# Optimization experiments

Hardware: AMD Instinct MI355X
Metric: run time of the kernel (lower is better)

Reference implementation:

```python
import jax, jax.numpy as jnp
import numpy as np

LEVELS = np.array([8, 5, 5, 5], dtype=np.int64)
BASIS = np.cumprod(np.concatenate([[1], LEVELS[:-1]])).astype(np.int64)  # [1,8,40,200]
N_E = int(np.prod(LEVELS))  # 1000
BN_EPS = 1e-5
BOUND_EPS = 1e-3


def setup_inputs() -> dict:
    key = jax.random.key(0)
    ks = jax.random.split(key, 3)
    B, C, T, E = 32, 512, 4096, 4
    return {
        "z": jax.random.normal(ks[0], (B, C, T), dtype=jnp.float32),
        "W_in": jax.random.normal(ks[1], (C, E), dtype=jnp.float32) * 0.05,
        "b_in": jnp.zeros((E,), dtype=jnp.float32),
        "gamma": jnp.ones((E,), dtype=jnp.float32),
        "beta": jnp.zeros((E,), dtype=jnp.float32),
        "W_out": jax.random.normal(ks[2], (E, C), dtype=jnp.float32) * 0.05,
        "b_out": jnp.zeros((C,), dtype=jnp.float32),
    }


def _round_ste(x):
    return x + jax.lax.stop_gradient(jnp.round(x) - x)


def reference(z, W_in, b_in, gamma, beta, W_out, b_out):
    levels = jnp.asarray(LEVELS, dtype=jnp.float32)      # [E]
    basis = jnp.asarray(BASIS, dtype=jnp.float32)        # [E]
    half_w = jnp.floor(levels / 2.0)                     # levels // 2
    B, C, T = z.shape
    N = B * T

    # preprocess: 'n c t -> (n t) c'
    x = jnp.transpose(z, (0, 2, 1)).reshape(N, C)        # [N, C]
    # project_in
    h = x @ W_in + b_in                                   # [N, E]
    # BatchNorm1d, training mode (biased batch stats)
    mu = jnp.mean(h, axis=0)
    var = jnp.var(h, axis=0)
    h = (h - mu) * jax.lax.rsqrt(var + BN_EPS) * gamma + beta

    # bound + round_ste quantize
    half_l = (levels - 1.0) * (1.0 - BOUND_EPS) / 2.0
    offset = jnp.where(jnp.mod(levels, 2.0) == 0.0, 0.5, 0.0)
    shift = jnp.tan(offset / half_l)
    bounded = jnp.tanh(h + shift) * half_l - offset
    zhat_n = _round_ste(bounded) / half_w                 # [N, E], normalized codes

    # codes -> indices
    idx = jnp.sum((zhat_n * half_w + half_w) * basis, axis=-1).astype(jnp.int32)  # [N]

    # project_out, '(b t) c -> b c t'
    out = zhat_n @ W_out + b_out                          # [N, C]
    zhat = jnp.transpose(out.reshape(B, T, C), (0, 2, 1))  # [B, C, T]

    commit_loss = jnp.mean((z - jax.lax.stop_gradient(zhat)) ** 2)

    # perplexity via counts (avoids [N, n_e] one-hot)
    counts = jnp.zeros((N_E,), dtype=jnp.float32).at[idx].add(1.0)
    e_mean = counts / N
    perplexity = jnp.exp(-jnp.sum(e_mean * jnp.log(e_mean + 1e-10)))

    return zhat, commit_loss, perplexity
```

## Files before the change

kernel.cpp:

```cpp
#include <hip/hip_runtime.h>
#include <math.h>


namespace {
constexpr int Cv = 512, Tv = 4096, Bv = 32;
constexpr int Nv = Bv * Tv;
constexpr long long TOTv = (long long)Nv * Cv;
constexpr int NBA = 512;
constexpr int NBC = 512;
constexpr int NCP = 128;

constexpr size_t OFF_H  = 0;
constexpr size_t OFF_G  = OFF_H  + (size_t)Nv * 16;
constexpr size_t OFF_BS = OFF_G  + (size_t)Nv * 16;
constexpr size_t OFF_CN = OFF_BS + (size_t)NBA * 10 * 8;
constexpr size_t OFF_CP = OFF_CN + 32 * 8;
constexpr size_t OFF_CT = OFF_CP + (size_t)NCP * 8;
}

__global__ __launch_bounds__(256, 2) void fsq_kA(
    const float* __restrict__ z, const float* __restrict__ W_in,
    const float* __restrict__ b_in, const float* __restrict__ W_out,
    const float* __restrict__ b_out,
    float* __restrict__ h_ws, float* __restrict__ g_ws, double* __restrict__ bs)
{
    __shared__ float s_wi[512][4];
    __shared__ float s_wo[512][4];
    __shared__ float s_bo[512];
    __shared__ float red_h[4][256][4];
    __shared__ float red_g[4][256][4];
    __shared__ double s_st[4][10];

    const int tid = threadIdx.x;
    const int lane = tid & 63;
    const int w = tid >> 6;
    const int bid = blockIdx.x;
    const int b = bid >> 4;
    const int t0 = (bid & 15) << 8;

    for (int i = tid; i < 512; i += 256) {
        *(float4*)&s_wi[i][0] = *(const float4*)(W_in + i * 4);
        s_wo[i][0] = W_out[i];
        s_wo[i][1] = W_out[512 + i];
        s_wo[i][2] = W_out[1024 + i];
        s_wo[i][3] = W_out[1536 + i];
        s_bo[i] = b_out[i];
    }
    __syncthreads();

    float h[4][4] = {}, g[4][4] = {};
    float z2 = 0.f, zb = 0.f;
    const float* zp = z + (size_t)b * Cv * Tv + t0 + lane * 4;
#pragma unroll 4
    for (int ci = 0; ci < 128; ++ci) {
        const int c = ci * 4 + w;
        const float4 zv = *(const float4*)(zp + (size_t)c * Tv);
        const float4 wi = *(const float4*)&s_wi[c][0];
        const float4 wo = *(const float4*)&s_wo[c][0];
        const float bo = s_bo[c];
        const float zr[4] = {zv.x, zv.y, zv.z, zv.w};
#pragma unroll
        for (int j = 0; j < 4; ++j) {
            h[j][0] = fmaf(zr[j], wi.x, h[j][0]);
            h[j][1] = fmaf(zr[j], wi.y, h[j][1]);
            h[j][2] = fmaf(zr[j], wi.z, h[j][2]);
            h[j][3] = fmaf(zr[j], wi.w, h[j][3]);
            g[j][0] = fmaf(zr[j], wo.x, g[j][0]);
            g[j][1] = fmaf(zr[j], wo.y, g[j][1]);
            g[j][2] = fmaf(zr[j], wo.z, g[j][2]);
            g[j][3] = fmaf(zr[j], wo.w, g[j][3]);
            z2 = fmaf(zr[j], zr[j], z2);
        }
        zb = fmaf((zr[0] + zr[1]) + (zr[2] + zr[3]), bo, zb);
    }

#pragma unroll
    for (int j = 0; j < 4; ++j) {
        *(float4*)&red_h[w][lane * 4 + j][0] = make_float4(h[j][0], h[j][1], h[j][2], h[j][3]);
        *(float4*)&red_g[w][lane * 4 + j][0] = make_float4(g[j][0], g[j][1], g[j][2], g[j][3]);
    }
    __syncthreads();

    const float4 ra = *(const float4*)&red_h[0][tid][0];
    const float4 rb = *(const float4*)&red_h[1][tid][0];
    const float4 rc = *(const float4*)&red_h[2][tid][0];
    const float4 rd = *(const float4*)&red_h[3][tid][0];
    float hh[4];
    hh[0] = (ra.x + rb.x) + (rc.x + rd.x) + b_in[0];
    hh[1] = (ra.y + rb.y) + (rc.y + rd.y) + b_in[1];
    hh[2] = (ra.z + rb.z) + (rc.z + rd.z) + b_in[2];
    hh[3] = (ra.w + rb.w) + (rc.w + rd.w) + b_in[3];
    const float4 qa = *(const float4*)&red_g[0][tid][0];
    const float4 qb = *(const float4*)&red_g[1][tid][0];
    const float4 qc = *(const float4*)&red_g[2][tid][0];
    const float4 qd = *(const float4*)&red_g[3][tid][0];
    float gg[4];
    gg[0] = (qa.x + qb.x) + (qc.x + qd.x);
    gg[1] = (qa.y + qb.y) + (qc.y + qd.y);
    gg[2] = (qa.z + qb.z) + (qc.z + qd.z);
    gg[3] = (qa.w + qb.w) + (qc.w + qd.w);

    const int n = (b << 12) + t0 + tid;
    *(float4*)(h_ws + (size_t)n * 4) = make_float4(hh[0], hh[1], hh[2], hh[3]);
    *(float4*)(g_ws + (size_t)n * 4) = make_float4(gg[0], gg[1], gg[2], gg[3]);

    double st[10];
#pragma unroll
    for (int e = 0; e < 4; ++e) {
        st[e] = (double)hh[e];
        st[4 + e] = (double)hh[e] * (double)hh[e];
    }
    st[8] = (double)z2;
    st[9] = (double)zb;
#pragma unroll
    for (int k = 0; k < 10; ++k) {
#pragma unroll
        for (int m = 1; m < 64; m <<= 1) st[k] += __shfl_xor(st[k], m, 64);
    }
    if (lane == 0) {
#pragma unroll
        for (int k = 0; k < 10; ++k) s_st[w][k] = st[k];
    }
    __syncthreads();
    if (tid < 10)
        bs[(size_t)bid * 10 + tid] = (s_st[0][tid] + s_st[1][tid]) + (s_st[2][tid] + s_st[3][tid]);
}

__global__ __launch_bounds__(256) void fsq_kS(
    const float* __restrict__ gamma, const float* __restrict__ beta,
    const float* __restrict__ W_out, const float* __restrict__ b_out,
    const double* __restrict__ bs, double* __restrict__ consts,
    unsigned* __restrict__ counts)
{
    __shared__ double sbuf[15][256];
    const int tid = threadIdx.x;

    for (int i = tid; i < 1000; i += 256) counts[i] = 0;

    double a[10] = {};
    for (int r = tid; r < NBA; r += 256) {
        const double* p = bs + (size_t)r * 10;
#pragma unroll
        for (int k = 0; k < 10; ++k) a[k] += p[k];
    }
#pragma unroll
    for (int k = 0; k < 10; ++k) sbuf[k][tid] = a[k];
    __syncthreads();
    for (int s = 128; s > 0; s >>= 1) {
        if (tid < s) {
#pragma unroll
            for (int k = 0; k < 10; ++k) sbuf[k][tid] += sbuf[k][tid + s];
        }
        __syncthreads();
    }
    double tot[10];
    if (tid == 0) {
#pragma unroll
        for (int k = 0; k < 10; ++k) tot[k] = sbuf[k][0];
    }
    __syncthreads();

    double gr[15] = {};
    for (int c = tid; c < 512; c += 256) {
        const double w0 = (double)W_out[c], w1 = (double)W_out[512 + c];
        const double w2 = (double)W_out[1024 + c], w3 = (double)W_out[1536 + c];
        const double bb = (double)b_out[c];
        gr[0] += w0 * w0; gr[1] += w0 * w1; gr[2] += w0 * w2; gr[3] += w0 * w3;
        gr[4] += w1 * w1; gr[5] += w1 * w2; gr[6] += w1 * w3;
        gr[7] += w2 * w2; gr[8] += w2 * w3; gr[9] += w3 * w3;
        gr[10] += w0 * bb; gr[11] += w1 * bb; gr[12] += w2 * bb; gr[13] += w3 * bb;
        gr[14] += bb * bb;
    }
#pragma unroll
    for (int k = 0; k < 15; ++k) sbuf[k][tid] = gr[k];
    __syncthreads();
    for (int s = 128; s > 0; s >>= 1) {
        if (tid < s) {
#pragma unroll
            for (int k = 0; k < 15; ++k) sbuf[k][tid] += sbuf[k][tid + s];
        }
        __syncthreads();
    }
    if (tid == 0) {
        const double Ninv = 1.0 / (double)Nv;
#pragma unroll
        for (int e = 0; e < 4; ++e) {
            const double mu = tot[e] * Ninv;
            const double var = tot[4 + e] * Ninv - mu * mu;
            const double sc = (double)gamma[e] / sqrt(var + 1e-5);
            consts[e] = sc;
            consts[4 + e] = (double)beta[e] - mu * sc;
        }
        consts[8] = tot[8];
        consts[9] = tot[9];
#pragma unroll
        for (int k = 0; k < 15; ++k) consts[16 + k] = sbuf[k][0];
        constexpr double hl0 = (8.0 - 1.0) * (1.0 - 1e-3) / 2.0;
        consts[31] = tan(0.5 / hl0);
    }
}

__global__ __launch_bounds__(256, 2) void fsq_kC(
    const float* __restrict__ W_out, const float* __restrict__ b_out,
    const float* __restrict__ h_ws, const float* __restrict__ g_ws,
    const double* __restrict__ consts, unsigned* __restrict__ counts,
    double* __restrict__ cp, float* __restrict__ out)
{
    __shared__ float s_wo[128][4];
    __shared__ float s_bo[128];
    __shared__ double s_cp[4];

    const int tid = threadIdx.x;
    const int lane = tid & 63;
    const int w = tid >> 6;
    const int bid = blockIdx.x;
    const int b = bid >> 4;
    const int tt = (bid >> 2) & 3;
    const int cs = bid & 3;
    const int c0 = cs << 7;
    const int t0 = tt << 10;
    const int n0 = (b << 12) + t0;

    if (tid < 128) {
        const int c = c0 + tid;
        s_wo[tid][0] = W_out[c];
        s_wo[tid][1] = W_out[512 + c];
        s_wo[tid][2] = W_out[1024 + c];
        s_wo[tid][3] = W_out[1536 + c];
        s_bo[tid] = b_out[c];
    }
    __syncthreads();

    const double sc0 = consts[0], sc1 = consts[1], sc2 = consts[2], sc3 = consts[3];
    const double bi0 = consts[4], bi1 = consts[5], bi2 = consts[6], bi3 = consts[7];
    const double shift0 = consts[31];
    constexpr double hl0 = (8.0 - 1.0) * (1.0 - 1e-3) / 2.0;
    constexpr double hl1 = (5.0 - 1.0) * (1.0 - 1e-3) / 2.0;

    float zn[4][4];
    double qsum = 0.0;
#pragma unroll
    for (int j = 0; j < 4; ++j) {
        const int n = n0 + tid * 4 + j;
        const float4 hv = *(const float4*)(h_ws + (size_t)n * 4);
        const double hn0 = fma((double)hv.x, sc0, bi0);
        const double hn1 = fma((double)hv.y, sc1, bi1);
        const double hn2 = fma((double)hv.z, sc2, bi2);
        const double hn3 = fma((double)hv.w, sc3, bi3);
        const double r0 = rint(tanh(hn0 + shift0) * hl0 - 0.5);
        const double r1 = rint(tanh(hn1) * hl1);
        const double r2 = rint(tanh(hn2) * hl1);
        const double r3 = rint(tanh(hn3) * hl1);
        const double zd0 = r0 * 0.25, zd1 = r1 * 0.5, zd2 = r2 * 0.5, zd3 = r3 * 0.5;
        zn[j][0] = (float)zd0; zn[j][1] = (float)zd1;
        zn[j][2] = (float)zd2; zn[j][3] = (float)zd3;
        if (cs == 0) {
            const int code = ((int)r0 + 4) + ((int)r1 + 2) * 8 + ((int)r2 + 2) * 40
                           + ((int)r3 + 2) * 200;
            atomicAdd(&counts[code], 1u);
            const float4 gv = *(const float4*)(g_ws + (size_t)n * 4);
            const double cg = zd0 * (double)gv.x + zd1 * (double)gv.y
                            + zd2 * (double)gv.z + zd3 * (double)gv.w;
            double q = consts[16 + 14]
                     + 2.0 * (zd0 * consts[16 + 10] + zd1 * consts[16 + 11]
                            + zd2 * consts[16 + 12] + zd3 * consts[16 + 13])
                     + zd0 * zd0 * consts[16 + 0] + zd1 * zd1 * consts[16 + 4]
                     + zd2 * zd2 * consts[16 + 7] + zd3 * zd3 * consts[16 + 9]
                     + 2.0 * (zd0 * zd1 * consts[16 + 1] + zd0 * zd2 * consts[16 + 2]
                            + zd0 * zd3 * consts[16 + 3] + zd1 * zd2 * consts[16 + 5]
                            + zd1 * zd3 * consts[16 + 6] + zd2 * zd3 * consts[16 + 8]);
            qsum += q - 2.0 * cg;
        }
    }

#pragma unroll
    for (int m = 1; m < 64; m <<= 1) qsum += __shfl_xor(qsum, m, 64);
    if (lane == 0) s_cp[w] = qsum;
    __syncthreads();
    if (tid == 0 && cs == 0)
        cp[b * 4 + tt] = (s_cp[0] + s_cp[1]) + (s_cp[2] + s_cp[3]);

    float* op = out + ((size_t)b * Cv + c0) * Tv + t0 + tid * 4;
#pragma unroll 4
    for (int i = 0; i < 128; ++i) {
        const float4 wo = *(const float4*)&s_wo[i][0];
        const float bo = s_bo[i];
        float4 o;
        o.x = fmaf(zn[0][0], wo.x, fmaf(zn[0][1], wo.y,
              fmaf(zn[0][2], wo.z, fmaf(zn[0][3], wo.w, bo))));
        o.y = fmaf(zn[1][0], wo.x, fmaf(zn[1][1], wo.y,
              fmaf(zn[1][2], wo.z, fmaf(zn[1][3], wo.w, bo))));
        o.z = fmaf(zn[2][0], wo.x, fmaf(zn[2][1], wo.y,
              fmaf(zn[2][2], wo.z, fmaf(zn[2][3], wo.w, bo))));
        o.w = fmaf(zn[3][0], wo.x, fmaf(zn[3][1], wo.y,
              fmaf(zn[3][2], wo.z, fmaf(zn[3][3], wo.w, bo))));
        *(float4*)(op + (size_t)i * Tv) = o;
    }
}

__global__ __launch_bounds__(256) void fsq_kD(
    const double* __restrict__ cp, const double* __restrict__ consts,
    const unsigned* __restrict__ counts, float* __restrict__ out, int out_size)
{
    __shared__ double r1[256], r2[256];
    const int tid = threadIdx.x;
    double c_ = (tid < NCP) ? cp[tid] : 0.0;
    double pl = 0.0;
    for (int i = tid; i < 1000; i += 256) {
        const double em = (double)counts[i] / (double)Nv;
        pl += em * log(em + 1e-10);
    }
    r1[tid] = c_; r2[tid] = pl;
    __syncthreads();
    for (int s = 128; s > 0; s >>= 1) {
        if (tid < s) { r1[tid] += r1[tid + s]; r2[tid] += r2[tid + s]; }
        __syncthreads();
    }
    if (tid == 0) {
        const double commit = (consts[8] - 2.0 * consts[9] + r1[0]) / (double)TOTv;
        out[out_size - 2] = (float)commit;
        out[out_size - 1] = (float)exp(-r2[0]);
    }
}

extern "C" void kernel_launch(void* const* d_in, const int* in_sizes, int n_in,
                              void* d_out, int out_size, void* d_ws, size_t ws_size,
                              hipStream_t stream) {
    const float* z     = (const float*)d_in[0];
    const float* W_in  = (const float*)d_in[1];
    const float* b_in  = (const float*)d_in[2];
    const float* gamma = (const float*)d_in[3];
    const float* beta  = (const float*)d_in[4];
    const float* W_out = (const float*)d_in[5];
    const float* b_out = (const float*)d_in[6];
    float* out = (float*)d_out;

    char* ws = (char*)d_ws;
    float*    h_ws   = (float*)(ws + OFF_H);
    float*    g_ws   = (float*)(ws + OFF_G);
    double*   bs     = (double*)(ws + OFF_BS);
    double*   consts = (double*)(ws + OFF_CN);
    double*   cp     = (double*)(ws + OFF_CP);
    unsigned* counts = (unsigned*)(ws + OFF_CT);

    fsq_kA<<<NBA, 256, 0, stream>>>(z, W_in, b_in, W_out, b_out, h_ws, g_ws, bs);
    fsq_kS<<<1, 256, 0, stream>>>(gamma, beta, W_out, b_out, bs, consts, counts);
    fsq_kC<<<NBC, 256, 0, stream>>>(W_out, b_out, h_ws, g_ws, consts, counts, cp, out);
    fsq_kD<<<1, 256, 0, stream>>>(cp, consts, counts, out, out_size);
}
```

Baseline: 195.6 us.

## Split input projection over channel slices and decouple quantize from output projection

The first pass now splits the channel dimension into 8 slices per batch and runs 1024-thread blocks. Each block writes partial projections to workspace, and a new kernel reduces them and collects the BatchNorm statistics. Quantization moves into its own kernel, which stores compact 16-bit codes along with histogram counts and the loss terms. The output kernel decodes the codes into half-precision shared memory and streams out the projection, and the final scalar reduction is folded into its first block. The aim is more parallelism and better-shaped streaming during the read and write passes, at the cost of extra partial-sum traffic and one more launch.

```diff
diff --git a/kernel.cpp b/kernel.cpp
--- a/kernel.cpp
+++ b/kernel.cpp
@@ -1,4 +1,5 @@
 #include <hip/hip_runtime.h>
+#include <hip/hip_fp16.h>
 #include <math.h>
 
 
@@ -6,54 +7,53 @@
 constexpr int Cv = 512, Tv = 4096, Bv = 32;
 constexpr int Nv = Bv * Tv;
 constexpr long long TOTv = (long long)Nv * Cv;
-constexpr int NBA = 512;
-constexpr int NBC = 512;
-constexpr int NCP = 128;
-
-constexpr size_t OFF_H  = 0;
+constexpr int CSA = 8;
+constexpr int NBA = Bv * CSA;
+
+constexpr size_t OFF_HP = 0;
+constexpr size_t OFF_GP = OFF_HP + (size_t)NBA * Tv * 16;
+constexpr size_t OFF_H  = OFF_GP + (size_t)NBA * Tv * 16;
 constexpr size_t OFF_G  = OFF_H  + (size_t)Nv * 16;
-constexpr size_t OFF_BS = OFF_G  + (size_t)Nv * 16;
-constexpr size_t OFF_CN = OFF_BS + (size_t)NBA * 10 * 8;
+constexpr size_t OFF_B1 = OFF_G  + (size_t)Nv * 16;
+constexpr size_t OFF_B2 = OFF_B1 + 256 * 2 * 8;
+constexpr size_t OFF_CN = OFF_B2 + 512 * 8 * 8;
 constexpr size_t OFF_CP = OFF_CN + 32 * 8;
-constexpr size_t OFF_CT = OFF_CP + (size_t)NCP * 8;
-}
-
-__global__ __launch_bounds__(256, 2) void fsq_kA(
+constexpr size_t OFF_CT = OFF_CP + 512 * 8;
+constexpr size_t OFF_CD = OFF_CT + 4096;
+}
+
+__global__ __launch_bounds__(1024, 4) void fsq_kA(
     const float* __restrict__ z, const float* __restrict__ W_in,
-    const float* __restrict__ b_in, const float* __restrict__ W_out,
-    const float* __restrict__ b_out,
-    float* __restrict__ h_ws, float* __restrict__ g_ws, double* __restrict__ bs)
-{
-    __shared__ float s_wi[512][4];
-    __shared__ float s_wo[512][4];
-    __shared__ float s_bo[512];
-    __shared__ float red_h[4][256][4];
-    __shared__ float red_g[4][256][4];
-    __shared__ double s_st[4][10];
-
-    const int tid = threadIdx.x;
-    const int lane = tid & 63;
-    const int w = tid >> 6;
+    const float* __restrict__ W_out, const float* __restrict__ b_out,
+    float* __restrict__ h_part, float* __restrict__ g_part, double* __restrict__ bs1)
+{
+    __shared__ float s_wi[64][4];
+    __shared__ float s_wo[64][4];
+    __shared__ float s_bo[64];
+    __shared__ double red[2][1024];
+
+    const int tid = threadIdx.x;
     const int bid = blockIdx.x;
-    const int b = bid >> 4;
-    const int t0 = (bid & 15) << 8;
-
-    for (int i = tid; i < 512; i += 256) {
-        *(float4*)&s_wi[i][0] = *(const float4*)(W_in + i * 4);
-        s_wo[i][0] = W_out[i];
-        s_wo[i][1] = W_out[512 + i];
-        s_wo[i][2] = W_out[1024 + i];
-        s_wo[i][3] = W_out[1536 + i];
-        s_bo[i] = b_out[i];
+    const int b = bid >> 3;
+    const int cs = bid & 7;
+    const int c0 = cs << 6;
+
+    if (tid < 64) {
+        const int c = c0 + tid;
+        *(float4*)&s_wi[tid][0] = *(const float4*)(W_in + c * 4);
+        s_wo[tid][0] = W_out[c];
+        s_wo[tid][1] = W_out[512 + c];
+        s_wo[tid][2] = W_out[1024 + c];
+        s_wo[tid][3] = W_out[1536 + c];
+        s_bo[tid] = b_out[c];
     }
     __syncthreads();
 
     float h[4][4] = {}, g[4][4] = {};
     float z2 = 0.f, zb = 0.f;
-    const float* zp = z + (size_t)b * Cv * Tv + t0 + lane * 4;
+    const float* zp = z + ((size_t)b * Cv + c0) * Tv + tid * 4;
 #pragma unroll 4
-    for (int ci = 0; ci < 128; ++ci) {
-        const int c = ci * 4 + w;
+    for (int c = 0; c < 64; ++c) {
         const float4 zv = *(const float4*)(zp + (size_t)c * Tv);
         const float4 wi = *(const float4*)&s_wi[c][0];
         const float4 wo = *(const float4*)&s_wo[c][0];
@@ -74,63 +74,78 @@
         zb = fmaf((zr[0] + zr[1]) + (zr[2] + zr[3]), bo, zb);
     }
 
+    float* hp = h_part + ((size_t)bid * Tv + tid * 4) * 4;
+    float* gp = g_part + ((size_t)bid * Tv + tid * 4) * 4;
 #pragma unroll
     for (int j = 0; j < 4; ++j) {
-        *(float4*)&red_h[w][lane * 4 + j][0] = make_float4(h[j][0], h[j][1], h[j][2], h[j][3]);
-        *(float4*)&red_g[w][lane * 4 + j][0] = make_float4(g[j][0], g[j][1], g[j][2], g[j][3]);
-    }
-    __syncthreads();
-
-    const float4 ra = *(const float4*)&red_h[0][tid][0];
-    const float4 rb = *(const float4*)&red_h[1][tid][0];
-    const float4 rc = *(const float4*)&red_h[2][tid][0];
-    const float4 rd = *(const float4*)&red_h[3][tid][0];
-    float hh[4];
-    hh[0] = (ra.x + rb.x) + (rc.x + rd.x) + b_in[0];
-    hh[1] = (ra.y + rb.y) + (rc.y + rd.y) + b_in[1];
-    hh[2] = (ra.z + rb.z) + (rc.z + rd.z) + b_in[2];
-    hh[3] = (ra.w + rb.w) + (rc.w + rd.w) + b_in[3];
-    const float4 qa = *(const float4*)&red_g[0][tid][0];
-    const float4 qb = *(const float4*)&red_g[1][tid][0];
-    const float4 qc = *(const float4*)&red_g[2][tid][0];
-    const float4 qd = *(const float4*)&red_g[3][tid][0];
-    float gg[4];
-    gg[0] = (qa.x + qb.x) + (qc.x + qd.x);
-    gg[1] = (qa.y + qb.y) + (qc.y + qd.y);
-    gg[2] = (qa.z + qb.z) + (qc.z + qd.z);
-    gg[3] = (qa.w + qb.w) + (qc.w + qd.w);
-
-    const int n = (b << 12) + t0 + tid;
-    *(float4*)(h_ws + (size_t)n * 4) = make_float4(hh[0], hh[1], hh[2], hh[3]);
+        *(float4*)(hp + j * 4) = make_float4(h[j][0], h[j][1], h[j][2], h[j][3]);
+        *(float4*)(gp + j * 4) = make_float4(g[j][0], g[j][1], g[j][2], g[j][3]);
+    }
+
+    red[0][tid] = (double)z2;
+    red[1][tid] = (double)zb;
+    __syncthreads();
+    for (int s = 512; s > 0; s >>= 1) {
+        if (tid < s) { red[0][tid] += red[0][tid + s]; red[1][tid] += red[1][tid + s]; }
+        __syncthreads();
+    }
+    if (tid == 0) { bs1[bid * 2] = red[0][0]; bs1[bid * 2 + 1] = red[1][0]; }
+}
+
+__global__ __launch_bounds__(256) void fsq_kB(
+    const float* __restrict__ h_part, const float* __restrict__ g_part,
+    const float* __restrict__ b_in,
+    float* __restrict__ h_ws, float* __restrict__ g_ws, double* __restrict__ bs2)
+{
+    __shared__ double red[8][256];
+    const int tid = threadIdx.x;
+    const int bid = blockIdx.x;
+    const int b = bid >> 4;
+    const int t = ((bid & 15) << 8) + tid;
+    const int n = (b << 12) + t;
+
+    double hd[4];
+    hd[0] = (double)b_in[0]; hd[1] = (double)b_in[1];
+    hd[2] = (double)b_in[2]; hd[3] = (double)b_in[3];
+    float gg[4] = {0.f, 0.f, 0.f, 0.f};
+#pragma unroll
+    for (int cs = 0; cs < 8; ++cs) {
+        const size_t base = ((size_t)(b * 8 + cs) * Tv + t) * 4;
+        const float4 p = *(const float4*)(h_part + base);
+        const float4 q = *(const float4*)(g_part + base);
+        hd[0] += (double)p.x; hd[1] += (double)p.y;
+        hd[2] += (double)p.z; hd[3] += (double)p.w;
+        gg[0] += q.x; gg[1] += q.y; gg[2] += q.z; gg[3] += q.w;
+    }
+
+    *(float4*)(h_ws + (size_t)n * 4) =
+        make_float4((float)hd[0], (float)hd[1], (float)hd[2], (float)hd[3]);
     *(float4*)(g_ws + (size_t)n * 4) = make_float4(gg[0], gg[1], gg[2], gg[3]);
 
-    double st[10];
 #pragma unroll
     for (int e = 0; e < 4; ++e) {
-        st[e] = (double)hh[e];
-        st[4 + e] = (double)hh[e] * (double)hh[e];
-    }
-    st[8] = (double)z2;
-    st[9] = (double)zb;
-#pragma unroll
-    for (int k = 0; k < 10; ++k) {
-#pragma unroll
-        for (int m = 1; m < 64; m <<= 1) st[k] += __shfl_xor(st[k], m, 64);
-    }
-    if (lane == 0) {
-#pragma unroll
-        for (int k = 0; k < 10; ++k) s_st[w][k] = st[k];
-    }
-    __syncthreads();
-    if (tid < 10)
-        bs[(size_t)bid * 10 + tid] = (s_st[0][tid] + s_st[1][tid]) + (s_st[2][tid] + s_st[3][tid]);
+        red[e][tid] = hd[e];
+        red[4 + e][tid] = hd[e] * hd[e];
+    }
+    __syncthreads();
+    for (int s = 128; s > 0; s >>= 1) {
+        if (tid < s) {
+#pragma unroll
+            for (int k = 0; k < 8; ++k) red[k][tid] += red[k][tid + s];
+        }
+        __syncthreads();
+    }
+    if (tid == 0) {
+#pragma unroll
+        for (int k = 0; k < 8; ++k) bs2[bid * 8 + k] = red[k][0];
+    }
 }
 
 __global__ __launch_bounds__(256) void fsq_kS(
     const float* __restrict__ gamma, const float* __restrict__ beta,
     const float* __restrict__ W_out, const float* __restrict__ b_out,
-    const double* __restrict__ bs, double* __restrict__ consts,
-    unsigned* __restrict__ counts)
+    const double* __restrict__ bs1, const double* __restrict__ bs2,
+    double* __restrict__ consts, unsigned* __restrict__ counts)
 {
     __shared__ double sbuf[15][256];
     const int tid = threadIdx.x;
@@ -138,11 +153,13 @@
     for (int i = tid; i < 1000; i += 256) counts[i] = 0;
 
     double a[10] = {};
-    for (int r = tid; r < NBA; r += 256) {
-        const double* p = bs + (size_t)r * 10;
-#pragma unroll
-        for (int k = 0; k < 10; ++k) a[k] += p[k];
-    }
+    for (int r = tid; r < 512; r += 256) {
+        const double* p = bs2 + (size_t)r * 8;
+#pragma unroll
+        for (int k = 0; k < 8; ++k) a[k] += p[k];
+    }
+    a[8] = bs1[tid * 2];
+    a[9] = bs1[tid * 2 + 1];
 #pragma unroll
     for (int k = 0; k < 10; ++k) sbuf[k][tid] = a[k];
     __syncthreads();
@@ -200,28 +217,95 @@
     }
 }
 
-__global__ __launch_bounds__(256, 2) void fsq_kC(
-    const float* __restrict__ W_out, const float* __restrict__ b_out,
+__global__ __launch_bounds__(256) void fsq_kQ(
     const float* __restrict__ h_ws, const float* __restrict__ g_ws,
     const double* __restrict__ consts, unsigned* __restrict__ counts,
-    double* __restrict__ cp, float* __restrict__ out)
-{
-    __shared__ float s_wo[128][4];
-    __shared__ float s_bo[128];
+    unsigned short* __restrict__ codes, double* __restrict__ cp)
+{
     __shared__ double s_cp[4];
-
     const int tid = threadIdx.x;
     const int lane = tid & 63;
     const int w = tid >> 6;
+    const int n = blockIdx.x * 256 + tid;
+
+    const double sc0 = consts[0], sc1 = consts[1], sc2 = consts[2], sc3 = consts[3];
+    const double bi0 = consts[4], bi1 = consts[5], bi2 = consts[6], bi3 = consts[7];
+    const double shift0 = consts[31];
+    constexpr double hl0 = (8.0 - 1.0) * (1.0 - 1e-3) / 2.0;
+    constexpr double hl1 = (5.0 - 1.0) * (1.0 - 1e-3) / 2.0;
+
+    const float4 hv = *(const float4*)(h_ws + (size_t)n * 4);
+    const double hn0 = fma((double)hv.x, sc0, bi0);
+    const double hn1 = fma((double)hv.y, sc1, bi1);
+    const double hn2 = fma((double)hv.z, sc2, bi2);
+    const double hn3 = fma((double)hv.w, sc3, bi3);
+    const double r0 = rint(tanh(hn0 + shift0) * hl0 - 0.5);
+    const double r1 = rint(tanh(hn1) * hl1);
+    const double r2 = rint(tanh(hn2) * hl1);
+    const double r3 = rint(tanh(hn3) * hl1);
+    const double zd0 = r0 * 0.25, zd1 = r1 * 0.5, zd2 = r2 * 0.5, zd3 = r3 * 0.5;
+
+    const int code = ((int)r0 + 4) + ((int)r1 + 2) * 8 + ((int)r2 + 2) * 40
+                   + ((int)r3 + 2) * 200;
+    codes[n] = (unsigned short)code;
+    atomicAdd(&counts[code], 1u);
+
+    const float4 gv = *(const float4*)(g_ws + (size_t)n * 4);
+    const double cg = zd0 * (double)gv.x + zd1 * (double)gv.y
+                    + zd2 * (double)gv.z + zd3 * (double)gv.w;
+    double q = consts[16 + 14]
+             + 2.0 * (zd0 * consts[16 + 10] + zd1 * consts[16 + 11]
+                    + zd2 * consts[16 + 12] + zd3 * consts[16 + 13])
+             + zd0 * zd0 * consts[16 + 0] + zd1 * zd1 * consts[16 + 4]
+             + zd2 * zd2 * consts[16 + 7] + zd3 * zd3 * consts[16 + 9]
+             + 2.0 * (zd0 * zd1 * consts[16 + 1] + zd0 * zd2 * consts[16 + 2]
+                    + zd0 * zd3 * consts[16 + 3] + zd1 * zd2 * consts[16 + 5]
+                    + zd1 * zd3 * consts[16 + 6] + zd2 * zd3 * consts[16 + 8]);
+    double qsum = q - 2.0 * cg;
+#pragma unroll
+    for (int m = 1; m < 64; m <<= 1) qsum += __shfl_xor(qsum, m, 64);
+    if (lane == 0) s_cp[w] = qsum;
+    __syncthreads();
+    if (tid == 0) cp[blockIdx.x] = (s_cp[0] + s_cp[1]) + (s_cp[2] + s_cp[3]);
+}
+
+__global__ __launch_bounds__(256, 4) void fsq_kW(
+    const unsigned short* __restrict__ codes, const float* __restrict__ W_out,
+    const float* __restrict__ b_out, const double* __restrict__ cp,
+    const double* __restrict__ consts, const unsigned* __restrict__ counts,
+    float* __restrict__ out, int out_size)
+{
+    __shared__ __half2 s_zn[4096][2];
+    __shared__ float s_wo[32][4];
+    __shared__ float s_bo[32];
+    __shared__ double r1[256], r2[256];
+
+    const int tid = threadIdx.x;
     const int bid = blockIdx.x;
     const int b = bid >> 4;
-    const int tt = (bid >> 2) & 3;
-    const int cs = bid & 3;
-    const int c0 = cs << 7;
-    const int t0 = tt << 10;
-    const int n0 = (b << 12) + t0;
-
-    if (tid < 128) {
+    const int c0 = (bid & 15) << 5;
+
+    if (bid == 0) {
+        double c_ = cp[tid] + cp[tid + 256];
+        double pl = 0.0;
+        for (int i = tid; i < 1000; i += 256) {
+            const double em = (double)counts[i] / (double)Nv;
+            pl += em * log(em + 1e-10);
+        }
+        r1[tid] = c_; r2[tid] = pl;
+        __syncthreads();
+        for (int s = 128; s > 0; s >>= 1) {
+            if (tid < s) { r1[tid] += r1[tid + s]; r2[tid] += r2[tid + s]; }
+            __syncthreads();
+        }
+        if (tid == 0) {
+            out[out_size - 2] = (float)((consts[8] - 2.0 * consts[9] + r1[0]) / (double)TOTv);
+            out[out_size - 1] = (float)exp(-r2[0]);
+        }
+        __syncthreads();
+    }
+
+    if (tid < 32) {
         const int c = c0 + tid;
         s_wo[tid][0] = W_out[c];
         s_wo[tid][1] = W_out[512 + c];
@@ -229,97 +313,43 @@
         s_wo[tid][3] = W_out[1536 + c];
         s_bo[tid] = b_out[c];
     }
-    __syncthreads();
-
-    const double sc0 = consts[0], sc1 = consts[1], sc2 = consts[2], sc3 = consts[3];
-    const double bi0 = consts[4], bi1 = consts[5], bi2 = consts[6], bi3 = consts[7];
-    const double shift0 = consts[31];
-    constexpr double hl0 = (8.0 - 1.0) * (1.0 - 1e-3) / 2.0;
-    constexpr double hl1 = (5.0 - 1.0) * (1.0 - 1e-3) / 2.0;
-
-    float zn[4][4];
-    double qsum = 0.0;
-#pragma unroll
-    for (int j = 0; j < 4; ++j) {
-        const int n = n0 + tid * 4 + j;
-        const float4 hv = *(const float4*)(h_ws + (size_t)n * 4);
-        const double hn0 = fma((double)hv.x, sc0, bi0);
-        const double hn1 = fma((double)hv.y, sc1, bi1);
-        const double hn2 = fma((double)hv.z, sc2, bi2);
-        const double hn3 = fma((double)hv.w, sc3, bi3);
-        const double r0 = rint(tanh(hn0 + shift0) * hl0 - 0.5);
-        const double r1 = rint(tanh(hn1) * hl1);
-        const double r2 = rint(tanh(hn2) * hl1);
-        const double r3 = rint(tanh(hn3) * hl1);
-        const double zd0 = r0 * 0.25, zd1 = r1 * 0.5, zd2 = r2 * 0.5, zd3 = r3 * 0.5;
-        zn[j][0] = (float)zd0; zn[j][1] = (float)zd1;
-        zn[j][2] = (float)zd2; zn[j][3] = (float)zd3;
-        if (cs == 0) {
-            const int code = ((int)r0 + 4) + ((int)r1 + 2) * 8 + ((int)r2 + 2) * 40
-                           + ((int)r3 + 2) * 200;
-            atomicAdd(&counts[code], 1u);
-            const float4 gv = *(const float4*)(g_ws + (size_t)n * 4);
-            const double cg = zd0 * (double)gv.x + zd1 * (double)gv.y
-                            + zd2 * (double)gv.z + zd3 * (double)gv.w;
-            double q = consts[16 + 14]
-                     + 2.0 * (zd0 * consts[16 + 10] + zd1 * consts[16 + 11]
-                            + zd2 * consts[16 + 12] + zd3 * consts[16 + 13])
-                     + zd0 * zd0 * consts[16 + 0] + zd1 * zd1 * consts[16 + 4]
-                     + zd2 * zd2 * consts[16 + 7] + zd3 * zd3 * consts[16 + 9]
-                     + 2.0 * (zd0 * zd1 * consts[16 + 1] + zd0 * zd2 * consts[16 + 2]
-                            + zd0 * zd3 * consts[16 + 3] + zd1 * zd2 * consts[16 + 5]
-                            + zd1 * zd3 * consts[16 + 6] + zd2 * zd3 * consts[16 + 8]);
-            qsum += q - 2.0 * cg;
-        }
-    }
-
-#pragma unroll
-    for (int m = 1; m < 64; m <<= 1) qsum += __shfl_xor(qsum, m, 64);
-    if (lane == 0) s_cp[w] = qsum;
-    __syncthreads();
-    if (tid == 0 && cs == 0)
-        cp[b * 4 + tt] = (s_cp[0] + s_cp[1]) + (s_cp[2] + s_cp[3]);
-
-    float* op = out + ((size_t)b * Cv + c0) * Tv + t0 + tid * 4;
-#pragma unroll 4
-    for (int i = 0; i < 128; ++i) {
-        const float4 wo = *(const float4*)&s_wo[i][0];
-        const float bo = s_bo[i];
-        float4 o;
-        o.x = fmaf(zn[0][0], wo.x, fmaf(zn[0][1], wo.y,
-              fmaf(zn[0][2], wo.z, fmaf(zn[0][3], wo.w, bo))));
-        o.y = fmaf(zn[1][0], wo.x, fmaf(zn[1][1], wo.y,
-              fmaf(zn[1][2], wo.z, fmaf(zn[1][3], wo.w, bo))));
-        o.z = fmaf(zn[2][0], wo.x, fmaf(zn[2][1], wo.y,
-              fmaf(zn[2][2], wo.z, fmaf(zn[2][3], wo.w, bo))));
-        o.w = fmaf(zn[3][0], wo.x, fmaf(zn[3][1], wo.y,
-              fmaf(zn[3][2], wo.z, fmaf(zn[3][3], wo.w, bo))));
-        *(float4*)(op + (size_t)i * Tv) = o;
-    }
-}
-
-__global__ __launch_bounds__(256) void fsq_kD(
-    const double* __restrict__ cp, const double* __restrict__ consts,
-    const unsigned* __restrict__ counts, float* __restrict__ out, int out_size)
-{
-    __shared__ double r1[256], r2[256];
-    const int tid = threadIdx.x;
-    double c_ = (tid < NCP) ? cp[tid] : 0.0;
-    double pl = 0.0;
-    for (int i = tid; i < 1000; i += 256) {
-        const double em = (double)counts[i] / (double)Nv;
-        pl += em * log(em + 1e-10);
-    }
-    r1[tid] = c_; r2[tid] = pl;
-    __syncthreads();
-    for (int s = 128; s > 0; s >>= 1) {
-        if (tid < s) { r1[tid] += r1[tid + s]; r2[tid] += r2[tid + s]; }
-        __syncthreads();
-    }
-    if (tid == 0) {
-        const double commit = (consts[8] - 2.0 * consts[9] + r1[0]) / (double)TOTv;
-        out[out_size - 2] = (float)commit;
-        out[out_size - 1] = (float)exp(-r2[0]);
+    for (int r = tid; r < 4096; r += 256) {
+        const int code = (int)codes[(b << 12) + r];
+        const int x0 = code & 7;
+        const int c1 = code >> 3;
+        const int x1 = c1 % 5;
+        const int c2 = c1 / 5;
+        const int x2 = c2 % 5;
+        const int x3 = c2 / 5;
+        const float zn0 = (float)(x0 - 4) * 0.25f;
+        const float zn1 = (float)(x1 - 2) * 0.5f;
+        const float zn2 = (float)(x2 - 2) * 0.5f;
+        const float zn3 = (float)(x3 - 2) * 0.5f;
+        s_zn[r][0] = __floats2half2_rn(zn0, zn1);
+        s_zn[r][1] = __floats2half2_rn(zn2, zn3);
+    }
+    __syncthreads();
+
+    const int w = tid >> 6;
+    const int lane = tid & 63;
+#pragma unroll
+    for (int cc = 0; cc < 8; ++cc) {
+        const int ci = w * 8 + cc;
+        const float4 wo = *(const float4*)&s_wo[ci][0];
+        const float bo = s_bo[ci];
+        float* op = out + ((size_t)b * Cv + (c0 + ci)) * Tv;
+        for (int it = 0; it < 16; ++it) {
+            const int t = it * 256 + lane * 4;
+            float4 o;
+#pragma unroll
+            for (int j = 0; j < 4; ++j) {
+                const float2 p01 = __half22float2(s_zn[t + j][0]);
+                const float2 p23 = __half22float2(s_zn[t + j][1]);
+                (&o.x)[j] = fmaf(p01.x, wo.x, fmaf(p01.y, wo.y,
+                            fmaf(p23.x, wo.z, fmaf(p23.y, wo.w, bo))));
+            }
+            *(float4*)(op + t) = o;
+        }
     }
 }
 
@@ -336,15 +366,20 @@
     float* out = (float*)d_out;
 
     char* ws = (char*)d_ws;
-    float*    h_ws   = (float*)(ws + OFF_H);
-    float*    g_ws   = (float*)(ws + OFF_G);
-    double*   bs     = (double*)(ws + OFF_BS);
-    double*   consts = (double*)(ws + OFF_CN);
-    double*   cp     = (double*)(ws + OFF_CP);
-    unsigned* counts = (unsigned*)(ws + OFF_CT);
-
-    fsq_kA<<<NBA, 256, 0, stream>>>(z, W_in, b_in, W_out, b_out, h_ws, g_ws, bs);
-    fsq_kS<<<1, 256, 0, stream>>>(gamma, beta, W_out, b_out, bs, consts, counts);
-    fsq_kC<<<NBC, 256, 0, stream>>>(W_out, b_out, h_ws, g_ws, consts, counts, cp, out);
-    fsq_kD<<<1, 256, 0, stream>>>(cp, consts, counts, out, out_size);
-}
+    float*          h_part = (float*)(ws + OFF_HP);
+    float*          g_part = (float*)(ws + OFF_GP);
+    float*          h_ws   = (float*)(ws + OFF_H);
+    float*          g_ws   = (float*)(ws + OFF_G);
+    double*         bs1    = (double*)(ws + OFF_B1);
+    double*         bs2    = (double*)(ws + OFF_B2);
+    double*         consts = (double*)(ws + OFF_CN);
+    double*         cp     = (double*)(ws + OFF_CP);
+    unsigned*       counts = (unsigned*)(ws + OFF_CT);
+    unsigned short* codes  = (unsigned short*)(ws + OFF_CD);
+
+    fsq_kA<<<NBA, 1024, 0, stream>>>(z, W_in, W_out, b_out, h_part, g_part, bs1);
+    fsq_kB<<<512, 256, 0, stream>>>(h_part, g_part, b_in, h_ws, g_ws, bs2);
+    fsq_kS<<<1, 256, 0, stream>>>(gamma, beta, W_out, b_out, bs1, bs2, consts, counts);
+    fsq_kQ<<<512, 256, 0, stream>>>(h_ws, g_ws, consts, counts, codes, cp);
+    fsq_kW<<<512, 256, 0, stream>>>(codes, W_out, b_out, cp, consts, counts, out, out_size);
+}
```

Result: slower. 276.7 us (+41.5%).
